# Performance work log

Measured on AMD Instinct MI355X. Metric: run time of the kernel, lower is better.

The kernel has to match this reference:

```python
import jax, jax.numpy as jnp
import numpy as np

EMBED = 1024
HEAD = 128

def setup_inputs() -> dict:
    key = jax.random.key(0)
    k1, k2, k3, k4 = jax.random.split(key, 4)
    x = jax.random.normal(k1, (8, 2048, EMBED), dtype=jnp.float32)
    s = 1.0 / np.sqrt(EMBED)
    Wk = jax.random.normal(k2, (EMBED, HEAD), dtype=jnp.float32) * s
    Wq = jax.random.normal(k3, (EMBED, HEAD), dtype=jnp.float32) * s
    Wv = jax.random.normal(k4, (EMBED, HEAD), dtype=jnp.float32) * s
    return {"x": x, "Wk": Wk, "Wq": Wq, "Wv": Wv}

def reference(x, Wk, Wq, Wv):
    # x: [B,T,E]; projections: [B,T,H]
    k = x @ Wk
    q = x @ Wq
    v = x @ Wv
    T = x.shape[1]
    # NOTE: original scales by 1/sqrt(embedding_size), not head_size
    scale = 1.0 / jnp.sqrt(jnp.asarray(EMBED, dtype=x.dtype))
    scores = jnp.einsum('bth,bsh->bts', q, k) * scale  # [B,T,T]
    causal = jnp.tril(jnp.ones((T, T), dtype=bool))
    scores = jnp.where(causal, scores, -jnp.inf)
    attn = jax.nn.softmax(scores, axis=-1)
    return jnp.einsum('bts,bsh->bth', attn, v)
```

## Files before the change

kernel.cpp:

```cpp
#include <hip/hip_runtime.h>
#include <math.h>

typedef short bf16x2 __attribute__((ext_vector_type(2)));
typedef short bf16x4 __attribute__((ext_vector_type(4)));
typedef short bf16x8 __attribute__((ext_vector_type(8)));
typedef float f32x4 __attribute__((ext_vector_type(4)));

#define EMBED 1024
#define HEAD 128
#define BATCH 8
#define SEQ 2048

__device__ __forceinline__ short f2bf(float f) {
  union { float f; unsigned u; } v;
  v.f = f;
  unsigned r = v.u + 0x7fffu + ((v.u >> 16) & 1u);
  return (short)(r >> 16);
}

__device__ __forceinline__ void async_copy16(const void* g, void* l) {
#if __has_builtin(__builtin_amdgcn_global_load_lds)
  __builtin_amdgcn_global_load_lds(
      (const __attribute__((address_space(1))) unsigned int*)g,
      (__attribute__((address_space(3))) unsigned int*)l, 16, 0, 0);
#else
  *(f32x4*)l = *(const f32x4*)g;
#endif
}

__global__ __launch_bounds__(384) void wtrans_kernel(
    const float* __restrict__ Wq, const float* __restrict__ Wk,
    const float* __restrict__ Wv, short* __restrict__ WT3) {
  int kc8 = blockIdx.x;
  int n = threadIdx.x;
  int mtx = n >> 7, h = n & 127;
  const float* W = (mtx == 0) ? Wq : ((mtx == 1) ? Wk : Wv);
  float scale = (mtx == 0) ? (1.4426950408889634f / 32.0f) : 1.0f;
  bf16x8 o;
#pragma unroll
  for (int j = 0; j < 8; j++)
    o[j] = f2bf(W[(size_t)(kc8 * 8 + j) * HEAD + h] * scale);
  *(bf16x8*)&WT3[(size_t)kc8 * 3072 + n * 8] = o;
}

#define MFMA_BF16(D, A, B) D = __builtin_amdgcn_mfma_f32_16x16x32_bf16(A, B, D, 0, 0, 0)

#define PROJ_BODY(IT, C0, C1, C2, C3, C4, C5, N0, N1, N2, N3, N4, N5)          \
  {                                                                            \
    int it_ = (IT);                                                            \
    __syncthreads();                                                           \
    if (it_ < 15) {                                                            \
      const short* bp_ = bptr + (it_ + 1) * 24576;                             \
      N0 = *(const bf16x8*)(bp_);                                              \
      N1 = *(const bf16x8*)(bp_ + 128);                                        \
      N2 = *(const bf16x8*)(bp_ + 256);                                        \
      N3 = *(const bf16x8*)(bp_ + 12288);                                      \
      N4 = *(const bf16x8*)(bp_ + 12288 + 128);                                \
      N5 = *(const bf16x8*)(bp_ + 12288 + 256);                                \
      bf16x8 w0_;                                                              \
      w0_[0] = f2bf(xr0[0]); w0_[1] = f2bf(xr0[1]);                            \
      w0_[2] = f2bf(xr0[2]); w0_[3] = f2bf(xr0[3]);                            \
      w0_[4] = f2bf(xr1[0]); w0_[5] = f2bf(xr1[1]);                            \
      w0_[6] = f2bf(xr1[2]); w0_[7] = f2bf(xr1[3]);                            \
      *(bf16x8*)&As[(it_ & 1) ^ 1][aoff] = w0_;                                \
      if (it_ < 14) {                                                          \
        xr0 = *(const f32x4*)(xbase + (it_ + 2) * 64);                         \
        xr1 = *(const f32x4*)(xbase + (it_ + 2) * 64 + 4);                     \
      }                                                                        \
    }                                                                          \
    {                                                                          \
      const short* as_ = &As[it_ & 1][0];                                      \
      bf16x8 a0_ = *(const bf16x8*)&as_[sub * 72 + quad * 8];                  \
      bf16x8 a1_ = *(const bf16x8*)&as_[(16 + sub) * 72 + quad * 8];           \
      bf16x8 a2_ = *(const bf16x8*)&as_[(32 + sub) * 72 + quad * 8];           \
      bf16x8 a3_ = *(const bf16x8*)&as_[(48 + sub) * 72 + quad * 8];           \
      MFMA_BF16(acc[0][0], a0_, C0); MFMA_BF16(acc[1][0], a1_, C0);            \
      MFMA_BF16(acc[2][0], a2_, C0); MFMA_BF16(acc[3][0], a3_, C0);            \
      MFMA_BF16(acc[0][1], a0_, C1); MFMA_BF16(acc[1][1], a1_, C1);            \
      MFMA_BF16(acc[2][1], a2_, C1); MFMA_BF16(acc[3][1], a3_, C1);            \
      MFMA_BF16(acc[0][2], a0_, C2); MFMA_BF16(acc[1][2], a1_, C2);            \
      MFMA_BF16(acc[2][2], a2_, C2); MFMA_BF16(acc[3][2], a3_, C2);            \
      a0_ = *(const bf16x8*)&as_[sub * 72 + 32 + quad * 8];                    \
      a1_ = *(const bf16x8*)&as_[(16 + sub) * 72 + 32 + quad * 8];             \
      a2_ = *(const bf16x8*)&as_[(32 + sub) * 72 + 32 + quad * 8];             \
      a3_ = *(const bf16x8*)&as_[(48 + sub) * 72 + 32 + quad * 8];             \
      MFMA_BF16(acc[0][0], a0_, C3); MFMA_BF16(acc[1][0], a1_, C3);            \
      MFMA_BF16(acc[2][0], a2_, C3); MFMA_BF16(acc[3][0], a3_, C3);            \
      MFMA_BF16(acc[0][1], a0_, C4); MFMA_BF16(acc[1][1], a1_, C4);            \
      MFMA_BF16(acc[2][1], a2_, C4); MFMA_BF16(acc[3][1], a3_, C4);            \
      MFMA_BF16(acc[0][2], a0_, C5); MFMA_BF16(acc[1][2], a1_, C5);            \
      MFMA_BF16(acc[2][2], a2_, C5); MFMA_BF16(acc[3][2], a3_, C5);            \
    }                                                                          \
  }

__global__ __launch_bounds__(512, 2) void proj_kernel(
    const float* __restrict__ x, const short* __restrict__ WT3,
    short* __restrict__ q, short* __restrict__ kG, short* __restrict__ vG) {
  __shared__ __align__(16) short As[2][64 * 72];
  int tid = threadIdx.x;
  int w = tid >> 6, lane = tid & 63, quad = lane >> 4, sub = lane & 15;
  int nw = w;
  int mt = blockIdx.x;
  int m0 = mt * 64;

  int arow = tid >> 3;
  int akq = (tid & 7) * 8;
  const float* xbase = x + (size_t)(m0 + arow) * EMBED + akq;
  int aoff = arow * 72 + akq;

  const short* bptr = WT3 + quad * 3072 + nw * 384 + sub * 8;

  f32x4 acc[4][3];
#pragma unroll
  for (int am = 0; am < 4; am++)
#pragma unroll
    for (int an = 0; an < 3; an++) acc[am][an] = (f32x4)(0.0f);

  {
    f32x4 x0 = *(const f32x4*)(xbase + 0);
    f32x4 x1 = *(const f32x4*)(xbase + 4);
    bf16x8 w0;
    w0[0]=f2bf(x0[0]); w0[1]=f2bf(x0[1]); w0[2]=f2bf(x0[2]); w0[3]=f2bf(x0[3]);
    w0[4]=f2bf(x1[0]); w0[5]=f2bf(x1[1]); w0[6]=f2bf(x1[2]); w0[7]=f2bf(x1[3]);
    *(bf16x8*)&As[0][aoff] = w0;
  }
  f32x4 xr0 = *(const f32x4*)(xbase + 64);
  f32x4 xr1 = *(const f32x4*)(xbase + 68);
  bf16x8 bA0, bA1, bA2, bA3, bA4, bA5;
  bf16x8 bB0, bB1, bB2, bB3, bB4, bB5;
  bA0 = *(const bf16x8*)(bptr);
  bA1 = *(const bf16x8*)(bptr + 128);
  bA2 = *(const bf16x8*)(bptr + 256);
  bA3 = *(const bf16x8*)(bptr + 12288);
  bA4 = *(const bf16x8*)(bptr + 12288 + 128);
  bA5 = *(const bf16x8*)(bptr + 12288 + 256);

  for (int it2 = 0; it2 < 16; it2 += 2) {
    PROJ_BODY(it2,     bA0, bA1, bA2, bA3, bA4, bA5, bB0, bB1, bB2, bB3, bB4, bB5);
    PROJ_BODY(it2 + 1, bB0, bB1, bB2, bB3, bB4, bB5, bA0, bA1, bA2, bA3, bA4, bA5);
  }

#pragma unroll
  for (int am = 0; am < 4; am++)
#pragma unroll
    for (int an = 0; an < 3; an++) {
      int g = nw * 3 + an;
      int hcol = (g & 7) * 16 + sub;
      if (g < 8) {
#pragma unroll
        for (int r = 0; r < 4; r++) {
          int m = m0 + am * 16 + quad * 4 + r;
          q[(size_t)m * HEAD + hcol] = f2bf(acc[am][an][r]);
        }
      } else if (g < 16) {
        size_t base = (size_t)(mt * 2 + (am >> 1)) * 4096 + (hcol >> 3) * 256 + (hcol & 7);
#pragma unroll
        for (int r = 0; r < 4; r++)
          kG[base + ((am & 1) * 16 + quad * 4 + r) * 8] = f2bf(acc[am][an][r]);
      } else {
        bf16x4 pv;
#pragma unroll
        for (int r = 0; r < 4; r++) pv[r] = f2bf(acc[am][an][r]);
        *(bf16x4*)&vG[(size_t)(mt * 2 + (am >> 1)) * 4096 +
                      ((am & 1) * 2 + (quad >> 1)) * 1024 +
                      hcol * 8 + (quad & 1) * 4] = pv;
      }
    }
}

__global__ __launch_bounds__(256, 4) void attn_kernel(
    const short* __restrict__ q, const short* __restrict__ kG,
    const short* __restrict__ vG, float* __restrict__ o_acc,
    float* __restrict__ l_acc) {
  __shared__ __align__(16) short Kb[2][4096];
  __shared__ __align__(16) short Vb[2][4096];
  __shared__ __align__(16) short Pb[4][16 * 40];
  int tid = threadIdx.x;
  int w = tid >> 6, lane = tid & 63, quad = lane >> 4, sub = lane & 15;
  int bx = blockIdx.x;
  int b = bx & 7;
  int v = 79 - (bx >> 3);
  int qt, c;
  if (v < 8)       { qt = v;                               c = 0; }
  else if (v < 24) { int i2 = v - 8;  qt = 8  + (i2 >> 1); c = i2 & 1; }
  else if (v < 48) { int i2 = v - 24; qt = 16 + i2 / 3;    c = i2 % 3; }
  else             { int i2 = v - 48; qt = 24 + (i2 >> 2); c = i2 & 3; }
  int q0 = qt * 64;
  int kb0 = c * 512;
  int len = min(512, q0 + 64 - kb0);
  int ntiles = len >> 5;

  const short* kp = kG + (size_t)b * SEQ * HEAD;
  const short* vp = vG + (size_t)b * SEQ * HEAD;
  int cc0 = tid, cc1 = tid + 256;

  bf16x8 qf[4];
  const short* qrow = q + (size_t)(b * SEQ + q0 + w * 16 + sub) * HEAD + quad * 8;
#pragma unroll
  for (int kc = 0; kc < 4; kc++) qf[kc] = *(const bf16x8*)(qrow + kc * 32);

  f32x4 o[8];
#pragma unroll
  for (int h = 0; h < 8; h++) o[h] = (f32x4)(0.0f);
  float l[4] = {0.0f, 0.0f, 0.0f, 0.0f};
  int wrow = q0 + w * 16;
  int qrq = wrow + quad * 4;

  {
    size_t blk = (size_t)(kb0 >> 5) * 4096;
    async_copy16(kp + blk + cc0 * 8, &Kb[0][cc0 * 8]);
    async_copy16(kp + blk + cc1 * 8, &Kb[0][cc1 * 8]);
    async_copy16(vp + blk + cc0 * 8, &Vb[0][cc0 * 8]);
    async_copy16(vp + blk + cc1 * 8, &Vb[0][cc1 * 8]);
  }

  for (int j = 0; j < ntiles; j++) {
    int kb = kb0 + j * 32;
    int cur = j & 1;
    __syncthreads();
    if (j + 1 < ntiles) {
      int nxt = cur ^ 1;
      size_t blk = (size_t)((kb + 32) >> 5) * 4096;
      async_copy16(kp + blk + cc0 * 8, &Kb[nxt][cc0 * 8]);
      async_copy16(kp + blk + cc1 * 8, &Kb[nxt][cc1 * 8]);
      async_copy16(vp + blk + cc0 * 8, &Vb[nxt][cc0 * 8]);
      async_copy16(vp + blk + cc1 * 8, &Vb[nxt][cc1 * 8]);
    }
    f32x4 s0 = (f32x4)(0.0f), s1 = (f32x4)(0.0f);
#pragma unroll
    for (int kk = 0; kk < 4; kk++) {
      bf16x8 f0 = *(const bf16x8*)&Kb[cur][((kk * 4 + quad) * 32 + sub) * 8];
      bf16x8 f1 = *(const bf16x8*)&Kb[cur][((kk * 4 + quad) * 32 + 16 + sub) * 8];
      s0 = __builtin_amdgcn_mfma_f32_16x16x32_bf16(qf[kk], f0, s0, 0, 0, 0);
      s1 = __builtin_amdgcn_mfma_f32_16x16x32_bf16(qf[kk], f1, s1, 0, 0, 0);
    }
    bool edge = (kb + 31 > wrow);
    float e0[4], e1[4];
#pragma unroll
    for (int r = 0; r < 4; r++) {
      e0[r] = __builtin_amdgcn_exp2f(s0[r]);
      e1[r] = __builtin_amdgcn_exp2f(s1[r]);
    }
    if (edge) {
#pragma unroll
      for (int r = 0; r < 4; r++) {
        if (kb + sub > qrq + r) e0[r] = 0.0f;
        if (kb + 16 + sub > qrq + r) e1[r] = 0.0f;
      }
    }
    short* pw = &Pb[w][0];
#pragma unroll
    for (int r = 0; r < 4; r++) {
      l[r] += e0[r] + e1[r];
      pw[(quad * 4 + r) * 40 + sub] = f2bf(e0[r]);
      pw[(quad * 4 + r) * 40 + sub + 16] = f2bf(e1[r]);
    }
    bf16x8 pa = *(const bf16x8*)&pw[sub * 40 + quad * 8];
#pragma unroll
    for (int h8 = 0; h8 < 8; h8++) {
      bf16x8 vf = *(const bf16x8*)&Vb[cur][(quad * 128 + h8 * 16 + sub) * 8];
      o[h8] = __builtin_amdgcn_mfma_f32_16x16x32_bf16(pa, vf, o[h8], 0, 0, 0);
    }
  }

  float* ob = o_acc + (size_t)(b * SEQ + qrq) * HEAD + sub;
#pragma unroll
  for (int r = 0; r < 4; r++)
#pragma unroll
    for (int h8 = 0; h8 < 8; h8++)
      unsafeAtomicAdd(ob + (size_t)r * HEAD + h8 * 16, o[h8][r]);
#pragma unroll
  for (int r = 0; r < 4; r++) {
#pragma unroll
    for (int off = 1; off < 16; off <<= 1) l[r] += __shfl_xor(l[r], off);
  }
  if (sub == 0) {
#pragma unroll
    for (int r = 0; r < 4; r++)
      unsafeAtomicAdd(&l_acc[b * SEQ + qrq + r], l[r]);
  }
}

__global__ __launch_bounds__(256) void norm_kernel(
    float* __restrict__ o, const float* __restrict__ l_acc) {
  int idx = blockIdx.x * 256 + threadIdx.x;
  f32x4 v = ((const f32x4*)o)[idx];
  float inv = 1.0f / l_acc[idx >> 5];
  v[0] *= inv; v[1] *= inv; v[2] *= inv; v[3] *= inv;
  ((f32x4*)o)[idx] = v;
}

extern "C" void kernel_launch(void* const* d_in, const int* in_sizes, int n_in,
                              void* d_out, int out_size, void* d_ws, size_t ws_size,
                              hipStream_t stream) {
  const float* x  = (const float*)d_in[0];
  const float* Wk = (const float*)d_in[1];
  const float* Wq = (const float*)d_in[2];
  const float* Wv = (const float*)d_in[3];
  char* ws = (char*)d_ws;
  short* WT3   = (short*)(ws);
  short* vG    = (short*)(ws + (size_t)1  * (1 << 20));
  short* q     = (short*)(ws + (size_t)5  * (1 << 20));
  short* kG    = (short*)(ws + (size_t)9  * (1 << 20));
  float* l_acc = (float*)(ws + (size_t)13 * (1 << 20));
  float* out   = (float*)d_out;

  hipMemsetAsync(out, 0, (size_t)BATCH * SEQ * HEAD * sizeof(float), stream);
  hipMemsetAsync(l_acc, 0, (size_t)BATCH * SEQ * sizeof(float), stream);
  wtrans_kernel<<<dim3(128), 384, 0, stream>>>(Wq, Wk, Wv, WT3);
  proj_kernel<<<dim3(256), 512, 0, stream>>>(x, WT3, q, kG, vG);
  attn_kernel<<<dim3(640), 256, 0, stream>>>(q, kG, vG, out, l_acc);
  norm_kernel<<<dim3(2048), 256, 0, stream>>>(out, l_acc);
}
```

Baseline: 158.2 us.

## Split projection kernel over column halves with 256-thread blocks

Projection work is split so each block computes half of the 384 output columns, with 512 blocks of 256 threads instead of 256 blocks of 512 threads. Each thread now loads and converts 16 x elements per stage instead of 8. This spreads work over more blocks to improve CU utilisation. In exchange, x is read and converted to bf16 twice, once per column half.

```diff
diff --git a/kernel.cpp b/kernel.cpp
--- a/kernel.cpp
+++ b/kernel.cpp
@@ -57,15 +57,23 @@
       N3 = *(const bf16x8*)(bp_ + 12288);                                      \
       N4 = *(const bf16x8*)(bp_ + 12288 + 128);                                \
       N5 = *(const bf16x8*)(bp_ + 12288 + 256);                                \
-      bf16x8 w0_;                                                              \
+      bf16x8 w0_, w1_;                                                         \
       w0_[0] = f2bf(xr0[0]); w0_[1] = f2bf(xr0[1]);                            \
       w0_[2] = f2bf(xr0[2]); w0_[3] = f2bf(xr0[3]);                            \
       w0_[4] = f2bf(xr1[0]); w0_[5] = f2bf(xr1[1]);                            \
       w0_[6] = f2bf(xr1[2]); w0_[7] = f2bf(xr1[3]);                            \
+      w1_[0] = f2bf(xr2[0]); w1_[1] = f2bf(xr2[1]);                            \
+      w1_[2] = f2bf(xr2[2]); w1_[3] = f2bf(xr2[3]);                            \
+      w1_[4] = f2bf(xr3[0]); w1_[5] = f2bf(xr3[1]);                            \
+      w1_[6] = f2bf(xr3[2]); w1_[7] = f2bf(xr3[3]);                            \
       *(bf16x8*)&As[(it_ & 1) ^ 1][aoff] = w0_;                                \
+      *(bf16x8*)&As[(it_ & 1) ^ 1][aoff + 8] = w1_;                            \
       if (it_ < 14) {                                                          \
-        xr0 = *(const f32x4*)(xbase + (it_ + 2) * 64);                         \
-        xr1 = *(const f32x4*)(xbase + (it_ + 2) * 64 + 4);                     \
+        const float* xp_ = xbase + (it_ + 2) * 64;                             \
+        xr0 = *(const f32x4*)(xp_);                                            \
+        xr1 = *(const f32x4*)(xp_ + 4);                                        \
+        xr2 = *(const f32x4*)(xp_ + 8);                                        \
+        xr3 = *(const f32x4*)(xp_ + 12);                                       \
       }                                                                        \
     }                                                                          \
     {                                                                          \
@@ -93,22 +101,23 @@
     }                                                                          \
   }
 
-__global__ __launch_bounds__(512, 2) void proj_kernel(
+__global__ __launch_bounds__(256, 2) void proj_kernel(
     const float* __restrict__ x, const short* __restrict__ WT3,
     short* __restrict__ q, short* __restrict__ kG, short* __restrict__ vG) {
   __shared__ __align__(16) short As[2][64 * 72];
   int tid = threadIdx.x;
   int w = tid >> 6, lane = tid & 63, quad = lane >> 4, sub = lane & 15;
-  int nw = w;
-  int mt = blockIdx.x;
+  int bx = blockIdx.x;
+  int mt = bx & 255;
+  int nh = bx >> 8;
   int m0 = mt * 64;
 
-  int arow = tid >> 3;
-  int akq = (tid & 7) * 8;
+  int arow = tid >> 2;
+  int akq = (tid & 3) * 16;
   const float* xbase = x + (size_t)(m0 + arow) * EMBED + akq;
   int aoff = arow * 72 + akq;
 
-  const short* bptr = WT3 + quad * 3072 + nw * 384 + sub * 8;
+  const short* bptr = WT3 + quad * 3072 + (nh * 192 + w * 48 + sub) * 8;
 
   f32x4 acc[4][3];
 #pragma unroll
@@ -119,13 +128,20 @@
   {
     f32x4 x0 = *(const f32x4*)(xbase + 0);
     f32x4 x1 = *(const f32x4*)(xbase + 4);
-    bf16x8 w0;
+    f32x4 x2 = *(const f32x4*)(xbase + 8);
+    f32x4 x3 = *(const f32x4*)(xbase + 12);
+    bf16x8 w0, w1;
     w0[0]=f2bf(x0[0]); w0[1]=f2bf(x0[1]); w0[2]=f2bf(x0[2]); w0[3]=f2bf(x0[3]);
     w0[4]=f2bf(x1[0]); w0[5]=f2bf(x1[1]); w0[6]=f2bf(x1[2]); w0[7]=f2bf(x1[3]);
+    w1[0]=f2bf(x2[0]); w1[1]=f2bf(x2[1]); w1[2]=f2bf(x2[2]); w1[3]=f2bf(x2[3]);
+    w1[4]=f2bf(x3[0]); w1[5]=f2bf(x3[1]); w1[6]=f2bf(x3[2]); w1[7]=f2bf(x3[3]);
     *(bf16x8*)&As[0][aoff] = w0;
+    *(bf16x8*)&As[0][aoff + 8] = w1;
   }
   f32x4 xr0 = *(const f32x4*)(xbase + 64);
   f32x4 xr1 = *(const f32x4*)(xbase + 68);
+  f32x4 xr2 = *(const f32x4*)(xbase + 72);
+  f32x4 xr3 = *(const f32x4*)(xbase + 76);
   bf16x8 bA0, bA1, bA2, bA3, bA4, bA5;
   bf16x8 bB0, bB1, bB2, bB3, bB4, bB5;
   bA0 = *(const bf16x8*)(bptr);
@@ -144,7 +160,7 @@
   for (int am = 0; am < 4; am++)
 #pragma unroll
     for (int an = 0; an < 3; an++) {
-      int g = nw * 3 + an;
+      int g = nh * 12 + w * 3 + an;
       int hcol = (g & 7) * 16 + sub;
       if (g < 8) {
 #pragma unroll
@@ -308,7 +324,7 @@
   hipMemsetAsync(out, 0, (size_t)BATCH * SEQ * HEAD * sizeof(float), stream);
   hipMemsetAsync(l_acc, 0, (size_t)BATCH * SEQ * sizeof(float), stream);
   wtrans_kernel<<<dim3(128), 384, 0, stream>>>(Wq, Wk, Wv, WT3);
-  proj_kernel<<<dim3(256), 512, 0, stream>>>(x, WT3, q, kG, vG);
+  proj_kernel<<<dim3(512), 256, 0, stream>>>(x, WT3, q, kG, vG);
   attn_kernel<<<dim3(640), 256, 0, stream>>>(q, kG, vG, out, l_acc);
   norm_kernel<<<dim3(2048), 256, 0, stream>>>(out, l_acc);
 }
```

New measurement: 154.0 us (median of 2 runs). 2.6% less time.
